# Performance work log

Hardware: AMD Instinct MI355X
Metric: run time of the kernel (lower is better)

## Reference

```python
import jax, jax.numpy as jnp
import numpy as np

N = 20000       # nodes
E = 160000      # edges (avg degree 8)
NFEAT = 512
NHID = 512
NCLASS = 64
NLAYERS = 4


def setup_inputs() -> dict:
    key = jax.random.key(0)
    ks = jax.random.split(key, 9)
    s = 0.05
    x = jax.random.normal(ks[0], (N, NFEAT), dtype=jnp.float32)
    edge_index = jax.random.randint(ks[1], (2, E), 0, N, dtype=jnp.int64)
    W_enc = jax.random.normal(ks[2], (NFEAT, NHID), dtype=jnp.float32) * s
    b_enc = jnp.zeros((NHID,), dtype=jnp.float32)
    W_convs = jax.random.normal(ks[3], (NLAYERS, NHID, NHID), dtype=jnp.float32) * s
    b_convs = jnp.zeros((NLAYERS, NHID), dtype=jnp.float32)
    W_dec = jax.random.normal(ks[4], (NHID, NCLASS), dtype=jnp.float32) * s
    b_dec = jnp.zeros((NCLASS,), dtype=jnp.float32)
    return {"x": x, "edge_index": edge_index, "W_enc": W_enc, "b_enc": b_enc,
            "W_convs": W_convs, "b_convs": b_convs, "W_dec": W_dec, "b_dec": b_dec}


def reference(x, edge_index, W_enc, b_enc, W_convs, b_convs, W_dec, b_dec):
    n = x.shape[0]
    loops = jnp.arange(n, dtype=edge_index.dtype)
    # GCNConv adds self-loops, then sym-normalizes: D^-1/2 (A+I) D^-1/2
    src = jnp.concatenate([edge_index[0], loops])  # [E+N]
    dst = jnp.concatenate([edge_index[1], loops])  # [E+N]
    deg = jax.ops.segment_sum(jnp.ones_like(dst, dtype=x.dtype), dst, num_segments=N)
    dinv = jnp.where(deg > 0, jax.lax.rsqrt(deg), jnp.zeros_like(deg))
    norm = (dinv[src] * dinv[dst])[:, None]  # [E+N, 1]

    # encoder: relu(Linear)
    h = jax.nn.relu(x @ W_enc + b_enc)

    def gcn_step(h, wb):
        W, b = wb
        hW = h @ W                                   # [N, H]
        msg = hW[src] * norm                         # gather + scale
        agg = jax.ops.segment_sum(msg, dst, num_segments=N)  # scatter-add
        return jax.nn.relu(agg + b), None            # bias after aggregation (PyG)

    h, _ = jax.lax.scan(gcn_step, h, (W_convs, b_convs))

    # decoder (dropout p=0 in eval -> identity)
    return h @ W_dec + b_dec
```

## Files before the change

### kernel.cpp

```cpp
#include <hip/hip_runtime.h>

#define N_NODES 20000
#define E_EDGES 160000
#define NFEAT   512
#define NHID    512
#define NCLASS  64
#define NLAYERS 4

#define SCAN_CHUNK 1024
#define NBLK ((N_NODES + SCAN_CHUNK - 1) / SCAN_CHUNK)

using bf16x8 = __attribute__((ext_vector_type(8))) short;
using f32x4  = __attribute__((ext_vector_type(4))) float;
using u16x8  = __attribute__((ext_vector_type(8))) unsigned short;

__device__ __forceinline__ unsigned short f2bf(float f) {
    union { float f; unsigned int u; } v; v.f = f;
    unsigned int u = v.u + 0x7FFFu + ((v.u >> 16) & 1u);
    return (unsigned short)(u >> 16);
}
__device__ __forceinline__ float bf2f(unsigned short h) {
    union { unsigned int u; float f; } v; v.u = ((unsigned int)h) << 16;
    return v.f;
}
__device__ __forceinline__ void gl2lds16(const void* gptr, void* lptr) {
    __builtin_amdgcn_global_load_lds(
        (const __attribute__((address_space(1))) unsigned int*)gptr,
        (__attribute__((address_space(3))) unsigned int*)lptr,
        16, 0, 0);
}


__global__ __launch_bounds__(256) void conv_f32_bf16(const float* __restrict__ in,
                                                     unsigned short* __restrict__ out,
                                                     int n4) {
    int i = blockIdx.x * 256 + threadIdx.x;
    if (i < n4) {
        float4 v = ((const float4*)in)[i];
        ushort4 o;
        o.x = f2bf(v.x); o.y = f2bf(v.y); o.z = f2bf(v.z); o.w = f2bf(v.w);
        ((ushort4*)out)[i] = o;
    }
}

__global__ __launch_bounds__(256) void transpose_all(const float* __restrict__ W_enc,
                                                     const float* __restrict__ W_convs,
                                                     const float* __restrict__ W_dec,
                                                     unsigned short* __restrict__ WencT,
                                                     unsigned short* __restrict__ WcvT,
                                                     unsigned short* __restrict__ WdecT) {
    __shared__ float tile[32][33];
    const int id = blockIdx.z;
    const float* W; unsigned short* WT; int N;
    const int K = 512;
    if (id == 0)                { W = W_enc; WT = WencT; N = NHID; }
    else if (id <= NLAYERS)     { W = W_convs + (size_t)(id - 1) * NHID * NHID;
                                  WT = WcvT  + (size_t)(id - 1) * NHID * NHID; N = NHID; }
    else                        { W = W_dec; WT = WdecT; N = NCLASS; }

    const int n0 = blockIdx.x * 32;
    if (n0 >= N) return;
    const int k0 = blockIdx.y * 32;
    const int tx = threadIdx.x & 31, ty = threadIdx.x >> 5;
#pragma unroll
    for (int i = 0; i < 32; i += 8)
        tile[ty + i][tx] = W[(size_t)(k0 + ty + i) * N + n0 + tx];
    __syncthreads();
#pragma unroll
    for (int i = 0; i < 32; i += 8)
        WT[(size_t)(n0 + ty + i) * K + k0 + tx] = f2bf(tile[tx][ty + i]);
}

__global__ __launch_bounds__(256) void csr_count(const int* __restrict__ dst,
                                                 int* __restrict__ counts) {
    int e = blockIdx.x * 256 + threadIdx.x;
    if (e < E_EDGES) atomicAdd(&counts[dst[e]], 1);
}

__global__ __launch_bounds__(256) void block_sums(const int* __restrict__ counts,
                                                  int* __restrict__ bsums) {
    __shared__ int red[256];
    const int b = blockIdx.x, t = threadIdx.x;
    const int base = b * SCAN_CHUNK + t * 4;
    int s = 0;
    if (base + 3 < N_NODES) {
        int4 v = *(const int4*)(counts + base);
        s = v.x + v.y + v.z + v.w;
    } else {
        for (int i = 0; i < 4; ++i)
            if (base + i < N_NODES) s += counts[base + i];
    }
    red[t] = s;
    __syncthreads();
    for (int off = 128; off > 0; off >>= 1) {
        if (t < off) red[t] += red[t + off];
        __syncthreads();
    }
    if (t == 0) bsums[b] = red[0];
}

__global__ __launch_bounds__(64) void scan_bsums(const int* __restrict__ bsums,
                                                 int* __restrict__ boffs) {
    const int t = threadIdx.x;
    const int orig = (t < NBLK) ? bsums[t] : 0;
    int v = orig;
    for (int off = 1; off < 64; off <<= 1) {
        int u = __shfl_up(v, off, 64);
        if (t >= off) v += u;
    }
    if (t < NBLK) boffs[t] = v - orig;
}

__global__ __launch_bounds__(256) void write_rowptr(const int* __restrict__ counts,
                                                    const int* __restrict__ boffs,
                                                    int* __restrict__ row_ptr,
                                                    int* __restrict__ cursor,
                                                    float* __restrict__ dinv) {
    __shared__ int part[256];
    const int b = blockIdx.x, t = threadIdx.x;
    const int base = b * SCAN_CHUNK + t * 4;
    int c[4], s = 0;
    for (int i = 0; i < 4; ++i) {
        int idx = base + i;
        c[i] = (idx < N_NODES) ? counts[idx] : 0;
        s += c[i];
    }
    part[t] = s;
    __syncthreads();
    for (int off = 1; off < 256; off <<= 1) {
        int v = (t >= off) ? part[t - off] : 0;
        __syncthreads();
        part[t] += v;
        __syncthreads();
    }
    int run = boffs[b] + ((t == 0) ? 0 : part[t - 1]);
    for (int i = 0; i < 4; ++i) {
        int idx = base + i;
        if (idx < N_NODES) {
            row_ptr[idx] = run;
            cursor[idx]  = run;
            dinv[idx]    = rsqrtf((float)c[i] + 1.0f);
            run += c[i];
        }
    }
    if (b == 0 && t == 0) row_ptr[N_NODES] = E_EDGES;
}

__global__ __launch_bounds__(256) void csr_fill(const int* __restrict__ src,
                                                const int* __restrict__ dst,
                                                const float* __restrict__ dinv,
                                                int* __restrict__ cursor,
                                                int* __restrict__ col,
                                                float* __restrict__ wgt) {
    int e = blockIdx.x * 256 + threadIdx.x;
    if (e < E_EDGES) {
        int s = src[e], d = dst[e];
        int pos = atomicAdd(&cursor[d], 1);
        col[pos] = s;
        wgt[pos] = dinv[s] * dinv[d];
    }
}

template <int BN, bool RELU, bool HASBIAS, bool OUTBF16>
__global__ __launch_bounds__(256) void gemm_mfma(const unsigned short* __restrict__ A,
                                                 const unsigned short* __restrict__ BT,
                                                 const float* __restrict__ bias,
                                                 void* __restrict__ Cout,
                                                 int M, int N, int K) {
    constexpr int BM = 128, BK = 32;
    constexpr int R = (BN == 128) ? 4 : 2;
    constexpr int C = 4;
    __shared__ unsigned short lA[BM * BK];
    __shared__ unsigned short lB[BN * BK];

    const int t    = threadIdx.x;
    const int lane = t & 63;
    const int wv   = t >> 6;
    const int wr   = (BN == 128) ? (wv >> 1) : wv;
    const int wc   = (BN == 128) ? (wv & 1) : 0;
    const int lm   = lane & 15;
    const int quad = lane >> 4;

    const int m0 = blockIdx.y * BM;
    const int n0 = blockIdx.x * BN;

    f32x4 acc[R][C] = {};

    for (int kt = 0; kt < K; kt += BK) {
#pragma unroll
        for (int i = 0; i < (BM * BK) / (256 * 8); ++i) {
            int idx = i * 256 + t;
            int row = idx >> 2;
            int kof = (idx & 3) << 3;
            int gr = m0 + row; if (gr >= M) gr = M - 1;
            gl2lds16(A + (size_t)gr * K + kt + kof, &lA[idx * 8]);
        }
#pragma unroll
        for (int i = 0; i < (BN * BK) / (256 * 8); ++i) {
            int idx = i * 256 + t;
            int row = idx >> 2;
            int kof = (idx & 3) << 3;
            gl2lds16(BT + (size_t)(n0 + row) * K + kt + kof, &lB[idx * 8]);
        }
        __syncthreads();

        bf16x8 af[R], bfr[C];
#pragma unroll
        for (int r = 0; r < R; ++r)
            af[r] = *(const bf16x8*)&lA[(wr * R * 16 + r * 16 + lm) * BK + quad * 8];
#pragma unroll
        for (int c = 0; c < C; ++c)
            bfr[c] = *(const bf16x8*)&lB[(wc * C * 16 + c * 16 + lm) * BK + quad * 8];
#pragma unroll
        for (int r = 0; r < R; ++r)
#pragma unroll
            for (int c = 0; c < C; ++c)
                acc[r][c] = __builtin_amdgcn_mfma_f32_16x16x32_bf16(af[r], bfr[c],
                                                                    acc[r][c], 0, 0, 0);
        __syncthreads();
    }

#pragma unroll
    for (int r = 0; r < R; ++r) {
#pragma unroll
        for (int c = 0; c < C; ++c) {
            const int colg = n0 + wc * C * 16 + c * 16 + lm;
            const float bb = HASBIAS ? bias[colg] : 0.0f;
            const int rowb = m0 + wr * R * 16 + r * 16 + quad * 4;
#pragma unroll
            for (int i = 0; i < 4; ++i) {
                const int rr = rowb + i;
                if (rr < M) {
                    float v = acc[r][c][i] + bb;
                    if (RELU) v = fmaxf(v, 0.0f);
                    if (OUTBF16)
                        ((unsigned short*)Cout)[(size_t)rr * N + colg] = f2bf(v);
                    else
                        ((float*)Cout)[(size_t)rr * N + colg] = v;
                }
            }
        }
    }
}

__global__ __launch_bounds__(256) void gcn_aggregate(const unsigned short* __restrict__ hW,
                                                     const int* __restrict__ row_ptr,
                                                     const int* __restrict__ col,
                                                     const float* __restrict__ wgt,
                                                     const float* __restrict__ dinv,
                                                     const float* __restrict__ bias,
                                                     unsigned short* __restrict__ out) {
    const int wv   = threadIdx.x >> 6;
    const int lane = threadIdx.x & 63;
    const int d    = blockIdx.x * 4 + wv;
    if (d >= N_NODES) return;
    const int beg = row_ptr[d];
    const int end = row_ptr[d + 1];
    const size_t foff = (size_t)lane * 8;

    const float di = dinv[d];
    const float sl = di * di;
    u16x8 sv = *(const u16x8*)(hW + (size_t)d * NHID + foff);
    float acc[8];
#pragma unroll
    for (int i = 0; i < 8; ++i) acc[i] = bf2f(sv[i]) * sl;

    for (int b0 = beg; b0 < end; b0 += 64) {
        const int nb   = min(64, end - b0);
        const int last = nb - 1;
        int   myc = 0;
        float myw = 0.0f;
        if (lane < nb) { myc = col[b0 + lane]; myw = wgt[b0 + lane]; }

        for (int j = 0; j < nb; j += 8) {
            int   s[8];
            float w[8];
            u16x8 v[8];
#pragma unroll
            for (int k = 0; k < 8; ++k) {
                const int jj = j + k;
                s[k] = __shfl(myc, jj <= last ? jj : last);
                w[k] = (jj <= last) ? __shfl(myw, jj) : 0.0f;
            }
#pragma unroll
            for (int k = 0; k < 8; ++k)
                v[k] = *(const u16x8*)(hW + (size_t)s[k] * NHID + foff);
#pragma unroll
            for (int k = 0; k < 8; ++k)
#pragma unroll
                for (int i = 0; i < 8; ++i)
                    acc[i] += bf2f(v[k][i]) * w[k];
        }
    }

    const float4 b0v = *(const float4*)(bias + foff);
    const float4 b1v = *(const float4*)(bias + foff + 4);
    u16x8 r;
    r[0] = f2bf(fmaxf(acc[0] + b0v.x, 0.0f));
    r[1] = f2bf(fmaxf(acc[1] + b0v.y, 0.0f));
    r[2] = f2bf(fmaxf(acc[2] + b0v.z, 0.0f));
    r[3] = f2bf(fmaxf(acc[3] + b0v.w, 0.0f));
    r[4] = f2bf(fmaxf(acc[4] + b1v.x, 0.0f));
    r[5] = f2bf(fmaxf(acc[5] + b1v.y, 0.0f));
    r[6] = f2bf(fmaxf(acc[6] + b1v.z, 0.0f));
    r[7] = f2bf(fmaxf(acc[7] + b1v.w, 0.0f));
    *(u16x8*)(out + (size_t)d * NHID + foff) = r;
}

extern "C" void kernel_launch(void* const* d_in, const int* in_sizes, int n_in,
                              void* d_out, int out_size, void* d_ws, size_t ws_size,
                              hipStream_t stream) {
    const float* x       = (const float*)d_in[0];
    const int*   ei      = (const int*)d_in[1];
    const float* W_enc   = (const float*)d_in[2];
    const float* b_enc   = (const float*)d_in[3];
    const float* W_convs = (const float*)d_in[4];
    const float* b_convs = (const float*)d_in[5];
    const float* W_dec   = (const float*)d_in[6];
    const float* b_dec   = (const float*)d_in[7];
    float* out = (float*)d_out;

    const int* src = ei;
    const int* dst = ei + E_EDGES;

    char* ws = (char*)d_ws;
    auto alloc = [&](size_t bytes) {
        char* p = ws;
        ws += (bytes + 255) / 256 * 256;
        return p;
    };
    float* dinv     = (float*)alloc(N_NODES * 4);
    int*   counts   = (int*)  alloc(N_NODES * 4);
    int*   row_ptr  = (int*)  alloc((N_NODES + 1) * 4);
    int*   cursor   = (int*)  alloc(N_NODES * 4);
    int*   bsums    = (int*)  alloc(NBLK * 4);
    int*   boffs    = (int*)  alloc(NBLK * 4);
    int*   colA     = (int*)  alloc(E_EDGES * 4);
    float* wgtA     = (float*)alloc(E_EDGES * 4);
    unsigned short* xbf   = (unsigned short*)alloc((size_t)N_NODES * NFEAT * 2);
    unsigned short* WencT = (unsigned short*)alloc((size_t)NFEAT * NHID * 2);
    unsigned short* WcvT  = (unsigned short*)alloc((size_t)NLAYERS * NHID * NHID * 2);
    unsigned short* WdecT = (unsigned short*)alloc((size_t)NHID * NCLASS * 2);
    unsigned short* B1    = (unsigned short*)alloc((size_t)N_NODES * NHID * 2);
    unsigned short* B2    = (unsigned short*)alloc((size_t)N_NODES * NHID * 2);

    hipMemsetAsync(counts, 0, N_NODES * sizeof(int), stream);
    csr_count<<<(E_EDGES + 255) / 256, 256, 0, stream>>>(dst, counts);
    block_sums<<<NBLK, 256, 0, stream>>>(counts, bsums);
    scan_bsums<<<1, 64, 0, stream>>>(bsums, boffs);
    write_rowptr<<<NBLK, 256, 0, stream>>>(counts, boffs, row_ptr, cursor, dinv);
    csr_fill<<<(E_EDGES + 255) / 256, 256, 0, stream>>>(src, dst, dinv, cursor, colA, wgtA);

    {
        int n4 = N_NODES * NFEAT / 4;
        conv_f32_bf16<<<(n4 + 255) / 256, 256, 0, stream>>>(x, xbf, n4);
    }
    transpose_all<<<dim3(16, 16, NLAYERS + 2), 256, 0, stream>>>(
        W_enc, W_convs, W_dec, WencT, WcvT, WdecT);

    const int MB = (N_NODES + 127) / 128;

    gemm_mfma<128, true, true, true><<<dim3(NHID / 128, MB), 256, 0, stream>>>(
        xbf, WencT, b_enc, B1, N_NODES, NHID, NFEAT);

    for (int L = 0; L < NLAYERS; ++L) {
        gemm_mfma<128, false, false, true><<<dim3(NHID / 128, MB), 256, 0, stream>>>(
            B1, WcvT + (size_t)L * NHID * NHID, nullptr, B2, N_NODES, NHID, NHID);
        gcn_aggregate<<<(N_NODES + 3) / 4, 256, 0, stream>>>(
            B2, row_ptr, colA, wgtA, dinv, b_convs + (size_t)L * NHID, B1);
    }

    gemm_mfma<64, false, true, false><<<dim3(NCLASS / 64, MB), 256, 0, stream>>>(
        B1, WdecT, b_dec, out, N_NODES, NCLASS, NHID);
}
```

Before: 378.0 us.

## Fuse preprocessing kernels, convert x in GEMM load, pack edges as int2

Merges degree counting, block-sum computation and weight transposes into one prep kernel, with per-block shared-memory bins replacing the separate block_sums pass. It drops the standalone f32-to-bf16 conversion of x by converting inside the encoder GEMM's A-tile load, at the cost of losing the async global-to-LDS path for that GEMM. Edge column and weight are packed into one int2 array, padded so the aggregation loop reads them directly per 8-edge chunk instead of using wave-wide loads and shuffles. Row bounds are made wave-uniform via readfirstlane. The trade is fewer launches and less memory traffic against a slower encoder GEMM load and extra per-edge loads.

```diff
diff --git a/kernel.cpp b/kernel.cpp
--- a/kernel.cpp
+++ b/kernel.cpp
@@ -9,6 +9,7 @@
 
 #define SCAN_CHUNK 1024
 #define NBLK ((N_NODES + SCAN_CHUNK - 1) / SCAN_CHUNK)
+#define CNT_BLOCKS ((E_EDGES + 255) / 256)
 
 using bf16x8 = __attribute__((ext_vector_type(8))) short;
 using f32x4  = __attribute__((ext_vector_type(4))) float;
@@ -30,38 +31,46 @@
         16, 0, 0);
 }
 
-
-__global__ __launch_bounds__(256) void conv_f32_bf16(const float* __restrict__ in,
-                                                     unsigned short* __restrict__ out,
-                                                     int n4) {
-    int i = blockIdx.x * 256 + threadIdx.x;
-    if (i < n4) {
-        float4 v = ((const float4*)in)[i];
-        ushort4 o;
-        o.x = f2bf(v.x); o.y = f2bf(v.y); o.z = f2bf(v.z); o.w = f2bf(v.w);
-        ((ushort4*)out)[i] = o;
-    }
-}
-
-__global__ __launch_bounds__(256) void transpose_all(const float* __restrict__ W_enc,
-                                                     const float* __restrict__ W_convs,
-                                                     const float* __restrict__ W_dec,
-                                                     unsigned short* __restrict__ WencT,
-                                                     unsigned short* __restrict__ WcvT,
-                                                     unsigned short* __restrict__ WdecT) {
+__global__ __launch_bounds__(256) void prep_all(const int* __restrict__ dst,
+                                                int* __restrict__ counts,
+                                                int* __restrict__ bsums,
+                                                const float* __restrict__ W_enc,
+                                                const float* __restrict__ W_convs,
+                                                const float* __restrict__ W_dec,
+                                                unsigned short* __restrict__ WencT,
+                                                unsigned short* __restrict__ WcvT,
+                                                unsigned short* __restrict__ WdecT) {
+    __shared__ int bins[NBLK];
     __shared__ float tile[32][33];
-    const int id = blockIdx.z;
+    const int b = blockIdx.x, t = threadIdx.x;
+
+    if (b < CNT_BLOCKS) {
+        if (t < NBLK) bins[t] = 0;
+        __syncthreads();
+        const int e = b * 256 + t;
+        if (e < E_EDGES) {
+            const int d = dst[e];
+            atomicAdd(&counts[d], 1);
+            atomicAdd(&bins[d >> 10], 1);
+        }
+        __syncthreads();
+        if (t < NBLK && bins[t]) atomicAdd(&bsums[t], bins[t]);
+        return;
+    }
+
+    const int bid = b - CNT_BLOCKS;
+    const int id  = bid >> 8;
+    const int rem = bid & 255;
+    const int n0  = (rem & 15) * 32;
+    const int k0  = (rem >> 4) * 32;
     const float* W; unsigned short* WT; int N;
     const int K = 512;
-    if (id == 0)                { W = W_enc; WT = WencT; N = NHID; }
-    else if (id <= NLAYERS)     { W = W_convs + (size_t)(id - 1) * NHID * NHID;
-                                  WT = WcvT  + (size_t)(id - 1) * NHID * NHID; N = NHID; }
-    else                        { W = W_dec; WT = WdecT; N = NCLASS; }
-
-    const int n0 = blockIdx.x * 32;
+    if (id == 0)            { W = W_enc; WT = WencT; N = NHID; }
+    else if (id <= NLAYERS) { W = W_convs + (size_t)(id - 1) * NHID * NHID;
+                              WT = WcvT  + (size_t)(id - 1) * NHID * NHID; N = NHID; }
+    else                    { W = W_dec; WT = WdecT; N = NCLASS; }
     if (n0 >= N) return;
-    const int k0 = blockIdx.y * 32;
-    const int tx = threadIdx.x & 31, ty = threadIdx.x >> 5;
+    const int tx = t & 31, ty = t >> 5;
 #pragma unroll
     for (int i = 0; i < 32; i += 8)
         tile[ty + i][tx] = W[(size_t)(k0 + ty + i) * N + n0 + tx];
@@ -69,34 +78,6 @@
 #pragma unroll
     for (int i = 0; i < 32; i += 8)
         WT[(size_t)(n0 + ty + i) * K + k0 + tx] = f2bf(tile[tx][ty + i]);
-}
-
-__global__ __launch_bounds__(256) void csr_count(const int* __restrict__ dst,
-                                                 int* __restrict__ counts) {
-    int e = blockIdx.x * 256 + threadIdx.x;
-    if (e < E_EDGES) atomicAdd(&counts[dst[e]], 1);
-}
-
-__global__ __launch_bounds__(256) void block_sums(const int* __restrict__ counts,
-                                                  int* __restrict__ bsums) {
-    __shared__ int red[256];
-    const int b = blockIdx.x, t = threadIdx.x;
-    const int base = b * SCAN_CHUNK + t * 4;
-    int s = 0;
-    if (base + 3 < N_NODES) {
-        int4 v = *(const int4*)(counts + base);
-        s = v.x + v.y + v.z + v.w;
-    } else {
-        for (int i = 0; i < 4; ++i)
-            if (base + i < N_NODES) s += counts[base + i];
-    }
-    red[t] = s;
-    __syncthreads();
-    for (int off = 128; off > 0; off >>= 1) {
-        if (t < off) red[t] += red[t + off];
-        __syncthreads();
-    }
-    if (t == 0) bsums[b] = red[0];
 }
 
 __global__ __launch_bounds__(64) void scan_bsums(const int* __restrict__ bsums,
@@ -150,19 +131,18 @@
                                                 const int* __restrict__ dst,
                                                 const float* __restrict__ dinv,
                                                 int* __restrict__ cursor,
-                                                int* __restrict__ col,
-                                                float* __restrict__ wgt) {
+                                                int2* __restrict__ ew) {
     int e = blockIdx.x * 256 + threadIdx.x;
     if (e < E_EDGES) {
         int s = src[e], d = dst[e];
         int pos = atomicAdd(&cursor[d], 1);
-        col[pos] = s;
-        wgt[pos] = dinv[s] * dinv[d];
-    }
-}
-
-template <int BN, bool RELU, bool HASBIAS, bool OUTBF16>
-__global__ __launch_bounds__(256) void gemm_mfma(const unsigned short* __restrict__ A,
+        ew[pos] = make_int2(s, __float_as_int(dinv[s] * dinv[d]));
+    }
+    if (e < 8) ew[E_EDGES + e] = make_int2(0, 0);
+}
+
+template <int BN, bool RELU, bool HASBIAS, bool OUTBF16, bool A32>
+__global__ __launch_bounds__(256) void gemm_mfma(const void* __restrict__ Aptr,
                                                  const unsigned short* __restrict__ BT,
                                                  const float* __restrict__ bias,
                                                  void* __restrict__ Cout,
@@ -193,7 +173,20 @@
             int row = idx >> 2;
             int kof = (idx & 3) << 3;
             int gr = m0 + row; if (gr >= M) gr = M - 1;
-            gl2lds16(A + (size_t)gr * K + kt + kof, &lA[idx * 8]);
+            if constexpr (!A32) {
+                gl2lds16((const unsigned short*)Aptr + (size_t)gr * K + kt + kof,
+                         &lA[idx * 8]);
+            } else {
+                const float* p = (const float*)Aptr + (size_t)gr * K + kt + kof;
+                float4 f0 = *(const float4*)p;
+                float4 f1 = *(const float4*)(p + 4);
+                u16x8 pk;
+                pk[0] = f2bf(f0.x); pk[1] = f2bf(f0.y);
+                pk[2] = f2bf(f0.z); pk[3] = f2bf(f0.w);
+                pk[4] = f2bf(f1.x); pk[5] = f2bf(f1.y);
+                pk[6] = f2bf(f1.z); pk[7] = f2bf(f1.w);
+                *(u16x8*)&lA[idx * 8] = pk;
+            }
         }
 #pragma unroll
         for (int i = 0; i < (BN * BK) / (256 * 8); ++i) {
@@ -245,17 +238,17 @@
 
 __global__ __launch_bounds__(256) void gcn_aggregate(const unsigned short* __restrict__ hW,
                                                      const int* __restrict__ row_ptr,
-                                                     const int* __restrict__ col,
-                                                     const float* __restrict__ wgt,
+                                                     const int2* __restrict__ ew,
                                                      const float* __restrict__ dinv,
                                                      const float* __restrict__ bias,
                                                      unsigned short* __restrict__ out) {
     const int wv   = threadIdx.x >> 6;
     const int lane = threadIdx.x & 63;
-    const int d    = blockIdx.x * 4 + wv;
+    int d = blockIdx.x * 4 + wv;
+    d = __builtin_amdgcn_readfirstlane(d);
     if (d >= N_NODES) return;
-    const int beg = row_ptr[d];
-    const int end = row_ptr[d + 1];
+    const int beg = __builtin_amdgcn_readfirstlane(row_ptr[d]);
+    const int end = __builtin_amdgcn_readfirstlane(row_ptr[d + 1]);
     const size_t foff = (size_t)lane * 8;
 
     const float di = dinv[d];
@@ -265,32 +258,26 @@
 #pragma unroll
     for (int i = 0; i < 8; ++i) acc[i] = bf2f(sv[i]) * sl;
 
-    for (int b0 = beg; b0 < end; b0 += 64) {
-        const int nb   = min(64, end - b0);
-        const int last = nb - 1;
-        int   myc = 0;
-        float myw = 0.0f;
-        if (lane < nb) { myc = col[b0 + lane]; myw = wgt[b0 + lane]; }
-
-        for (int j = 0; j < nb; j += 8) {
-            int   s[8];
-            float w[8];
-            u16x8 v[8];
-#pragma unroll
-            for (int k = 0; k < 8; ++k) {
-                const int jj = j + k;
-                s[k] = __shfl(myc, jj <= last ? jj : last);
-                w[k] = (jj <= last) ? __shfl(myw, jj) : 0.0f;
-            }
-#pragma unroll
-            for (int k = 0; k < 8; ++k)
-                v[k] = *(const u16x8*)(hW + (size_t)s[k] * NHID + foff);
-#pragma unroll
-            for (int k = 0; k < 8; ++k)
-#pragma unroll
-                for (int i = 0; i < 8; ++i)
-                    acc[i] += bf2f(v[k][i]) * w[k];
-        }
+    for (int j = beg; j < end; j += 8) {
+        int   sK[8];
+        float wK[8];
+        u16x8 v[8];
+#pragma unroll
+        for (int k = 0; k < 8; ++k) {
+            const int jj = j + k;
+            const int2 e = ew[jj];
+            const bool valid = jj < end;
+            sK[k] = valid ? e.x : 0;
+            wK[k] = valid ? __int_as_float(e.y) : 0.0f;
+        }
+#pragma unroll
+        for (int k = 0; k < 8; ++k)
+            v[k] = *(const u16x8*)(hW + (size_t)sK[k] * NHID + foff);
+#pragma unroll
+        for (int k = 0; k < 8; ++k)
+#pragma unroll
+            for (int i = 0; i < 8; ++i)
+                acc[i] += bf2f(v[k][i]) * wK[k];
     }
 
     const float4 b0v = *(const float4*)(bias + foff);
@@ -330,46 +317,37 @@
         return p;
     };
     float* dinv     = (float*)alloc(N_NODES * 4);
-    int*   counts   = (int*)  alloc(N_NODES * 4);
+    int*   counts   = (int*)  alloc((N_NODES + NBLK) * 4);
+    int*   bsums    = counts + N_NODES;
     int*   row_ptr  = (int*)  alloc((N_NODES + 1) * 4);
     int*   cursor   = (int*)  alloc(N_NODES * 4);
-    int*   bsums    = (int*)  alloc(NBLK * 4);
     int*   boffs    = (int*)  alloc(NBLK * 4);
-    int*   colA     = (int*)  alloc(E_EDGES * 4);
-    float* wgtA     = (float*)alloc(E_EDGES * 4);
-    unsigned short* xbf   = (unsigned short*)alloc((size_t)N_NODES * NFEAT * 2);
+    int2*  ew       = (int2*) alloc((E_EDGES + 8) * 8);
     unsigned short* WencT = (unsigned short*)alloc((size_t)NFEAT * NHID * 2);
     unsigned short* WcvT  = (unsigned short*)alloc((size_t)NLAYERS * NHID * NHID * 2);
     unsigned short* WdecT = (unsigned short*)alloc((size_t)NHID * NCLASS * 2);
     unsigned short* B1    = (unsigned short*)alloc((size_t)N_NODES * NHID * 2);
     unsigned short* B2    = (unsigned short*)alloc((size_t)N_NODES * NHID * 2);
 
-    hipMemsetAsync(counts, 0, N_NODES * sizeof(int), stream);
-    csr_count<<<(E_EDGES + 255) / 256, 256, 0, stream>>>(dst, counts);
-    block_sums<<<NBLK, 256, 0, stream>>>(counts, bsums);
+    hipMemsetAsync(counts, 0, (N_NODES + NBLK) * sizeof(int), stream);
+    prep_all<<<CNT_BLOCKS + 6 * 256, 256, 0, stream>>>(
+        dst, counts, bsums, W_enc, W_convs, W_dec, WencT, WcvT, WdecT);
     scan_bsums<<<1, 64, 0, stream>>>(bsums, boffs);
     write_rowptr<<<NBLK, 256, 0, stream>>>(counts, boffs, row_ptr, cursor, dinv);
-    csr_fill<<<(E_EDGES + 255) / 256, 256, 0, stream>>>(src, dst, dinv, cursor, colA, wgtA);
-
-    {
-        int n4 = N_NODES * NFEAT / 4;
-        conv_f32_bf16<<<(n4 + 255) / 256, 256, 0, stream>>>(x, xbf, n4);
-    }
-    transpose_all<<<dim3(16, 16, NLAYERS + 2), 256, 0, stream>>>(
-        W_enc, W_convs, W_dec, WencT, WcvT, WdecT);
+    csr_fill<<<(E_EDGES + 255) / 256, 256, 0, stream>>>(src, dst, dinv, cursor, ew);
 
     const int MB = (N_NODES + 127) / 128;
 
-    gemm_mfma<128, true, true, true><<<dim3(NHID / 128, MB), 256, 0, stream>>>(
-        xbf, WencT, b_enc, B1, N_NODES, NHID, NFEAT);
+    gemm_mfma<128, true, true, true, true><<<dim3(NHID / 128, MB), 256, 0, stream>>>(
+        x, WencT, b_enc, B1, N_NODES, NHID, NFEAT);
 
     for (int L = 0; L < NLAYERS; ++L) {
-        gemm_mfma<128, false, false, true><<<dim3(NHID / 128, MB), 256, 0, stream>>>(
+        gemm_mfma<128, false, false, true, false><<<dim3(NHID / 128, MB), 256, 0, stream>>>(
             B1, WcvT + (size_t)L * NHID * NHID, nullptr, B2, N_NODES, NHID, NHID);
         gcn_aggregate<<<(N_NODES + 3) / 4, 256, 0, stream>>>(
-            B2, row_ptr, colA, wgtA, dinv, b_convs + (size_t)L * NHID, B1);
-    }
-
-    gemm_mfma<64, false, true, false><<<dim3(NCLASS / 64, MB), 256, 0, stream>>>(
+            B2, row_ptr, ew, dinv, b_convs + (size_t)L * NHID, B1);
+    }
+
+    gemm_mfma<64, false, true, false, false><<<dim3(NCLASS / 64, MB), 256, 0, stream>>>(
         B1, WdecT, b_dec, out, N_NODES, NCLASS, NHID);
 }
```

Result: faster. 363.2 us (-3.9%).
